# Kernel tuning notes

Hardware: AMD Instinct MI355X
Metric: run time of the kernel (lower is better)

The kernel has to match this reference:

```python
import jax, jax.numpy as jnp
import numpy as np

B, T, C = 2, 2048, 2048
NH, NKV, HD = 16, 8, 256
SOFTCAP = 50.0
ROPE_BASE = 10000.0


def setup_inputs() -> dict:
    key = jax.random.key(0)
    ks = jax.random.split(key, 5)
    s = 0.02
    return {
        "X": jax.random.normal(ks[0], (B, T, C), dtype=jnp.float32),
        "Wq": jax.random.normal(ks[1], (C, NH * HD), dtype=jnp.float32) * s,
        "Wk": jax.random.normal(ks[2], (C, NKV * HD), dtype=jnp.float32) * s,
        "Wv": jax.random.normal(ks[3], (C, NKV * HD), dtype=jnp.float32) * s,
        "Wo": jax.random.normal(ks[4], (NH * HD, C), dtype=jnp.float32) * s,
    }


def _rotate_half(x):
    x1, x2 = x[..., : x.shape[-1] // 2], x[..., x.shape[-1] // 2 :]
    return jnp.concatenate((-x2, x1), axis=-1)


def _rope_cos_sin(t, head_dim, dtype):
    inv_freq = 1.0 / ROPE_BASE ** (
        jnp.arange(0, head_dim, 2, dtype=jnp.int32).astype(jnp.float32) / head_dim
    )  # [HD/2]
    pos = jnp.arange(t, dtype=jnp.float32)  # [T]
    freqs = pos[:, None] * inv_freq[None, :]  # [T, HD/2]
    emb = jnp.concatenate((freqs, freqs), axis=-1)  # [T, HD]
    # shape [1, 1, T, HD] to broadcast over (B, H, T, HD)
    return (
        jnp.cos(emb).astype(dtype)[None, None],
        jnp.sin(emb).astype(dtype)[None, None],
    )


def reference(X, Wq, Wk, Wv, Wo):
    b, t, c = X.shape
    n_rep = NH // NKV

    q = (X @ Wq).reshape(b, t, NH, HD).transpose(0, 2, 1, 3)   # [B,NH,T,HD]
    k = (X @ Wk).reshape(b, t, NKV, HD).transpose(0, 2, 1, 3)  # [B,NKV,T,HD]
    v = (X @ Wv).reshape(b, t, NKV, HD).transpose(0, 2, 1, 3)

    cos, sin = _rope_cos_sin(t, HD, X.dtype)
    q = q * cos + _rotate_half(q) * sin
    k = k * cos + _rotate_half(k) * sin

    # repeat_kv (GQA): [B,NKV,T,HD] -> [B,NH,T,HD]
    k = jnp.repeat(k, n_rep, axis=1)
    v = jnp.repeat(v, n_rep, axis=1)

    scale = 256.0 ** (-0.5)  # hardcoded in source
    att = jnp.einsum("bhqd,bhkd->bhqk", q, k) * scale
    # tanh logit softcapping
    att = SOFTCAP * jnp.tanh(att / SOFTCAP)
    # causal mask
    causal = jnp.tril(jnp.ones((t, t), dtype=bool))
    att = jnp.where(causal[None, None], att, -jnp.inf)
    att = jax.nn.softmax(att, axis=-1)

    y = jnp.einsum("bhqk,bhkd->bhqd", att, v)  # [B,NH,T,HD]
    y = y.transpose(0, 2, 1, 3).reshape(b, t, NH * HD)
    return y @ Wo
```

## Files before the change

### kernel.cpp

```cpp
#include <hip/hip_runtime.h>
#include <hip/hip_bf16.h>

#define NHD 16
#define NKVH 8
#define HDIM 256
#define TSEQ 2048
#define BATCH 2

typedef unsigned int   u32;
typedef unsigned short u16;

typedef __attribute__((ext_vector_type(8))) short bf16x8;
typedef __attribute__((ext_vector_type(4))) float floatx4;

__device__ inline u32 cvt2bf(float lo, float hi) {
  u32 r;
  asm("v_cvt_pk_bf16_f32 %0, %1, %2" : "=v"(r) : "v"(lo), "v"(hi));
  return r;
}
__device__ inline u16 f2bf(float f) {
  union { float f; u32 i; } v; v.f = f;
  u32 r = v.i + 0x7fffu + ((v.i >> 16) & 1u);
  return (u16)(r >> 16);
}
__device__ inline float bf2f(u16 u) {
  union { u32 i; float f; } v; v.i = ((u32)u) << 16; return v.f;
}
__device__ inline float fexp2(float x) {
  float r; asm("v_exp_f32 %0, %1" : "=v"(r) : "v"(x)); return r;
}

typedef const __attribute__((address_space(1))) u32* gptr_t;
typedef __attribute__((address_space(3))) u32* lptr_t;
__device__ inline void gl_lds16(const void* g, void* l) {
  __builtin_amdgcn_global_load_lds((gptr_t)g, (lptr_t)l, 16, 0, 0);
}

__device__ inline void tconv_body(const float* __restrict__ in,
                                  u16* __restrict__ out, int R, int Cc,
                                  int bx, int by, int tid) {
  __shared__ float tile[64][65];
  const int r0 = by * 64, c0 = bx * 64;
  const int tr = tid >> 4;
  const int tc = (tid & 15) * 4;
#pragma unroll
  for (int j = 0; j < 4; ++j) {
    float4 v = *(const float4*)(in + (size_t)(r0 + tr + j * 16) * Cc + c0 + tc);
    tile[tr + j * 16][tc + 0] = v.x;
    tile[tr + j * 16][tc + 1] = v.y;
    tile[tr + j * 16][tc + 2] = v.z;
    tile[tr + j * 16][tc + 3] = v.w;
  }
  __syncthreads();
#pragma unroll
  for (int j = 0; j < 4; ++j) {
    int c = tr + j * 16;
    u16 o[4];
#pragma unroll
    for (int i = 0; i < 4; ++i) o[i] = f2bf(tile[tc + i][c]);
    *(uint2*)(out + (size_t)(c0 + c) * R + r0 + tc) = *(const uint2*)o;
  }
}

__global__ __launch_bounds__(256) void tconv_k(
    const float* __restrict__ in, u16* __restrict__ out, int R, int Cc)
{
  tconv_body(in, out, R, Cc, blockIdx.x, blockIdx.y, threadIdx.x);
}

__global__ __launch_bounds__(256) void xconv_k(
    const float* __restrict__ in, u16* __restrict__ out)
{
  size_t i = (size_t)blockIdx.x * 256 + threadIdx.x;
  float4 a = *(const float4*)(in + i * 8);
  float4 b = *(const float4*)(in + i * 8 + 4);
  uint4 o;
  o.x = cvt2bf(a.x, a.y); o.y = cvt2bf(a.z, a.w);
  o.z = cvt2bf(b.x, b.y); o.w = cvt2bf(b.z, b.w);
  *(uint4*)(out + i * 8) = o;
}

__global__ __launch_bounds__(256) void prep_k(
    const float* __restrict__ X,  const float* __restrict__ Wq,
    const float* __restrict__ Wk, const float* __restrict__ Wv,
    u16* __restrict__ XB, u16* __restrict__ WqT, u16* __restrict__ WkvT)
{
  const int bid = blockIdx.x, tid = threadIdx.x;
  if (bid < 4096) {
    size_t i = (size_t)bid * 256 + tid;
    float4 a = *(const float4*)(X + i * 8);
    float4 b = *(const float4*)(X + i * 8 + 4);
    uint4 o;
    o.x = cvt2bf(a.x, a.y); o.y = cvt2bf(a.z, a.w);
    o.z = cvt2bf(b.x, b.y); o.w = cvt2bf(b.z, b.w);
    *(uint4*)(XB + i * 8) = o;
  } else if (bid < 6144) {
    int idx = bid - 4096;
    tconv_body(Wq, WqT, 2048, 4096, idx & 63, idx >> 6, tid);
  } else if (bid < 7168) {
    int idx = bid - 6144;
    tconv_body(Wk, WkvT, 2048, 2048, idx & 31, idx >> 5, tid);
  } else {
    int idx = bid - 7168;
    tconv_body(Wv, WkvT + (size_t)2048 * 2048, 2048, 2048, idx & 31, idx >> 5, tid);
  }
}

template<int EPI, int BM>
__global__ __launch_bounds__(512, 2) void gemm256_k(
    const u16* __restrict__ Ab, const u16* __restrict__ BTp,
    void* __restrict__ Op, int M, int N, int K)
{
  constexpr int NI = BM / 32;
  constexpr int AI = BM / 64;
  __shared__ u16 LA[2][BM * 64];
  __shared__ u16 LB[2][256 * 64];
  const int t = threadIdx.x;
  const int lane = t & 63, wave = t >> 6;
  const int lg = lane >> 4, l15 = lane & 15;
  const int wm = wave >> 2, wn = wave & 3;
  const int mtiles = M / BM;
  const int mt = (int)blockIdx.x % mtiles, nt = (int)blockIdx.x / mtiles;
  const int m0 = mt * BM, n0 = nt << 8;

  const int arow = wave * (BM / 8) + (lane >> 3);
  const int ska  = ((lane & 7) ^ (arow & 7)) << 3;
  const int brow = wave * 32 + (lane >> 3);
  const int skb  = ((lane & 7) ^ (brow & 7)) << 3;
  const u16* Ag = Ab  + (size_t)(m0 + arow) * K + ska;
  const u16* Bg = BTp + (size_t)(n0 + brow) * K + skb;

  auto STAGE = [&](int k0, int sel) {
#pragma unroll
    for (int q = 0; q < AI; ++q)
      gl_lds16(Ag + k0 + (size_t)q * 8 * K, &LA[sel][(wave * (BM / 8) + q * 8) * 64]);
#pragma unroll
    for (int q = 0; q < 4; ++q)
      gl_lds16(Bg + k0 + (size_t)q * 8 * K, &LB[sel][(wave * 32 + q * 8) * 64]);
  };

  floatx4 acc[NI][4];
#pragma unroll
  for (int i = 0; i < NI; ++i)
#pragma unroll
    for (int j = 0; j < 4; ++j) acc[i][j] = (floatx4){0.f, 0.f, 0.f, 0.f};

  STAGE(0, 0);
  const int KT = K >> 6;
  for (int kt = 0; kt < KT; ++kt) {
    const int sel = kt & 1;
    if (kt + 1 < KT) {
      STAGE((kt + 1) << 6, sel ^ 1);
      if constexpr (BM == 256) asm volatile("s_waitcnt vmcnt(8)" ::: "memory");
      else                     asm volatile("s_waitcnt vmcnt(6)" ::: "memory");
    } else {
      asm volatile("s_waitcnt vmcnt(0)" ::: "memory");
    }
    __builtin_amdgcn_s_barrier();
    __builtin_amdgcn_sched_barrier(0);
    __builtin_amdgcn_s_setprio(1);
#pragma unroll
    for (int ks = 0; ks < 2; ++ks) {
      const int c = (ks << 2) + lg;
      bf16x8 bfv[4];
#pragma unroll
      for (int j = 0; j < 4; ++j) {
        int row = wn * 64 + (j << 4) + l15;
        bfv[j] = *(const bf16x8*)(&LB[sel][row * 64 + ((c ^ (row & 7)) << 3)]);
      }
#pragma unroll
      for (int i = 0; i < NI; ++i) {
        int row = wm * (BM / 2) + (i << 4) + l15;
        bf16x8 af = *(const bf16x8*)(&LA[sel][row * 64 + ((c ^ (row & 7)) << 3)]);
#pragma unroll
        for (int j = 0; j < 4; ++j)
          acc[i][j] = __builtin_amdgcn_mfma_f32_16x16x32_bf16(af, bfv[j], acc[i][j], 0, 0, 0);
      }
    }
    __builtin_amdgcn_s_setprio(0);
    __builtin_amdgcn_s_barrier();
  }

#pragma unroll
  for (int i = 0; i < NI; ++i) {
#pragma unroll
    for (int j = 0; j < 4; ++j) {
#pragma unroll
      for (int r = 0; r < 4; ++r) {
        int m = m0 + wm * (BM / 2) + (i << 4) + (lg << 2) + r;
        int n = n0 + wn * 64 + (j << 4) + l15;
        float v = acc[i][j][r];
        int bb = m >> 11, tt = m & 2047;
        if (EPI == 0) {
          ((float*)Op)[(size_t)m * N + n] = v;
        } else if (EPI == 1) {
          int h = n >> 8, d = n & 255;
          ((u16*)Op)[(((size_t)bb * NHD + h) * TSEQ + tt) * HDIM + d] = f2bf(v);
        } else {
          if (n < 2048) {
            int h = n >> 8, d = n & 255;
            ((u16*)Op)[(((size_t)bb * NKVH + h) * TSEQ + tt) * HDIM + d] = f2bf(v);
          } else {
            int n2 = n - 2048;
            int h = n2 >> 8, d = n2 & 255;
            ((u16*)Op)[8388608u + (((size_t)bb * NKVH + h) * HDIM + d) * TSEQ + tt] = f2bf(v);
          }
        }
      }
    }
  }
}

__global__ __launch_bounds__(256) void rope_k(u16* Qb, u16* Kb) {
  size_t idx = (size_t)blockIdx.x * 256 + threadIdx.x;
  const size_t qtot = (size_t)BATCH * NHD * TSEQ * 128;
  u16* buf;
  if (idx < qtot) buf = Qb;
  else { idx -= qtot; buf = Kb; }
  int d = (int)(idx & 127);
  size_t rest = idx >> 7;
  int tt = (int)(rest & (TSEQ - 1));
  float invf = exp2f(-(float)d * 0.103810253f);
  float th = (float)tt * invf;
  float sn, cs;
  sincosf(th, &sn, &cs);
  size_t base = rest * HDIM;
  float x1 = bf2f(buf[base + d]);
  float x2 = bf2f(buf[base + d + 128]);
  buf[base + d]       = f2bf(x1 * cs - x2 * sn);
  buf[base + d + 128] = f2bf(x2 * cs + x1 * sn);
}

__global__ __launch_bounds__(256, 2) void attn_k(
    const u16* __restrict__ Q, const u16* __restrict__ Kb,
    const u16* __restrict__ Vt, u16* __restrict__ Y)
{
  __shared__ u16 Ks2[2][32 * 256];
  __shared__ u16 Vs2[2][256 * 32];
  __shared__ u16 Ps[4 * 16 * 32];
  __shared__ float Ls[4][16];
  const int t = threadIdx.x, lane = t & 63, w = t >> 6;
  const int lg = lane >> 4, l15 = lane & 15;
  const int qt = 31 - (int)blockIdx.y;
  const int h = (int)blockIdx.x >> 1, b = (int)blockIdx.x & 1;
  const int hkv = h >> 1;

  const u16* Kg = Kb + ((size_t)(b * NKVH + hkv)) * TSEQ * HDIM;
  const u16* Vg = Vt + ((size_t)(b * NKVH + hkv)) * HDIM * TSEQ;

  int koff[4], voff[4];
#pragma unroll
  for (int q = 0; q < 4; ++q) {
    int krow = w * 8 + q * 2 + (lane >> 5);
    int kcc  = lane & 31;
    koff[q] = krow * 256 + ((kcc ^ (krow & 7)) << 3);
    int vd  = w * 64 + q * 16 + (lane >> 2);
    voff[q] = vd * TSEQ + (((lane & 3) ^ ((vd >> 2) & 3)) << 3);
  }

  auto STAGE = [&](int st, int sel) {
    const u16* kbase = Kg + (size_t)st * (32 * 256);
    const u16* vbase = Vg + st * 32;
#pragma unroll
    for (int q = 0; q < 4; ++q)
      gl_lds16(kbase + koff[q], &Ks2[sel][(w * 8 + q * 2) * 256]);
#pragma unroll
    for (int q = 0; q < 4; ++q)
      gl_lds16(vbase + voff[q], &Vs2[sel][(w * 64 + q * 16) * 32]);
  };

  const u16* Qg = Q + (((size_t)(b * NHD + h)) * TSEQ + qt * 64 + w * 16 + l15) * HDIM;
  bf16x8 qf[8];
#pragma unroll
  for (int ks = 0; ks < 8; ++ks) qf[ks] = *(const bf16x8*)(Qg + ks * 32 + lg * 8);

  floatx4 accY[16];
#pragma unroll
  for (int i = 0; i < 16; ++i) accY[i] = (floatx4){0.f, 0.f, 0.f, 0.f};
  float rsum = 0.f;

  const int qglob = qt * 64 + w * 16 + l15;
  const int qmaxw = qt * 64 + w * 16 + 15;
  const int nst = 2 * qt + 2;
  const int fps = (l15 ^ (l15 >> 2)) & 3;

  STAGE(0, 0);
  for (int st = 0; st < nst; ++st) {
    const int sel = st & 1;
    if (st + 1 < nst) {
      STAGE(st + 1, sel ^ 1);
      asm volatile("s_waitcnt vmcnt(8)" ::: "memory");
    } else {
      asm volatile("s_waitcnt vmcnt(0)" ::: "memory");
    }
    __builtin_amdgcn_s_barrier();
    __builtin_amdgcn_sched_barrier(0);

    if (st * 32 <= qmaxw) {
      __builtin_amdgcn_s_setprio(1);
#pragma unroll
      for (int stile = 0; stile < 2; ++stile) {
        floatx4 sa0 = (floatx4){0.f, 0.f, 0.f, 0.f};
        floatx4 sa1 = (floatx4){0.f, 0.f, 0.f, 0.f};
#pragma unroll
        for (int ks = 0; ks < 8; ++ks) {
          int row = (stile << 4) + l15;
          int c = (ks << 2) + lg;
          bf16x8 kf = *(const bf16x8*)((const char*)Ks2[sel] +
                        row * 512 + ((c ^ (row & 7)) << 4));
          if (ks & 1)
            sa1 = __builtin_amdgcn_mfma_f32_16x16x32_bf16(kf, qf[ks], sa1, 0, 0, 0);
          else
            sa0 = __builtin_amdgcn_mfma_f32_16x16x32_bf16(kf, qf[ks], sa0, 0, 0, 0);
        }
        int sbase = st * 32 + (stile << 4) + (lg << 2);
        float p[4];
#pragma unroll
        for (int r = 0; r < 4; ++r) {
          float s = sa0[r] + sa1[r];
          float tt = fmaf(s * s, -5.2083333e-7f, 1.0f);
          float pv = fexp2(s * 0.0901684403f * tt);
          pv = (sbase + r <= qglob) ? pv : 0.0f;
          p[r] = pv;
          rsum += pv;
        }
        uint2 pw;
        pw.x = cvt2bf(p[0], p[1]);
        pw.y = cvt2bf(p[2], p[3]);
        int o = (stile << 5) + (lg << 3);
        int gran = (o >> 4) ^ fps;
        *(uint2*)((char*)Ps + (w << 10) + l15 * 64 + (gran << 4) + (o & 15)) = pw;
      }
      {
        bf16x8 pf = *(const bf16x8*)((const char*)Ps + (w << 10) + l15 * 64 +
                      ((lg ^ fps) << 4));
#pragma unroll
        for (int dt = 0; dt < 16; ++dt) {
          int row = (dt << 4) + l15;
          bf16x8 vf = *(const bf16x8*)((const char*)Vs2[sel] +
                        row * 64 + ((lg ^ ((row >> 2) & 3)) << 4));
          accY[dt] = __builtin_amdgcn_mfma_f32_16x16x32_bf16(pf, vf, accY[dt], 0, 0, 0);
        }
      }
      __builtin_amdgcn_s_setprio(0);
    }
    __builtin_amdgcn_s_barrier();
  }

  rsum += __shfl_xor(rsum, 16);
  rsum += __shfl_xor(rsum, 32);
  if (lane < 16) Ls[w][l15] = rsum;
  __syncthreads();
  float inv[4];
#pragma unroll
  for (int r = 0; r < 4; ++r) inv[r] = 1.0f / Ls[w][(lg << 2) + r];

  u16* Yg = Y + ((size_t)(b * TSEQ + qt * 64 + w * 16)) * (NHD * HDIM) + h * HDIM;
#pragma unroll
  for (int dt = 0; dt < 16; ++dt)
#pragma unroll
    for (int r = 0; r < 4; ++r)
      Yg[(size_t)((lg << 2) + r) * (NHD * HDIM) + (dt << 4) + l15] =
          f2bf(accY[dt][r] * inv[r]);
}

extern "C" void kernel_launch(void* const* d_in, const int* in_sizes, int n_in,
                              void* d_out, int out_size, void* d_ws, size_t ws_size,
                              hipStream_t stream) {
  const float* X  = (const float*)d_in[0];
  const float* Wq = (const float*)d_in[1];
  const float* Wk = (const float*)d_in[2];
  const float* Wv = (const float*)d_in[3];
  const float* Wo = (const float*)d_in[4];
  float* out = (float*)d_out;

  u16* ws = (u16*)d_ws;
  dim3 blk(256);

  if (ws_size >= (size_t)117440512) {
    u16* XB   = ws;
    u16* WqT  = ws + 8388608;
    u16* WkvT = ws + 16777216;
    u16* Qb   = ws + 25165824;
    u16* KVb  = ws + 41943040;
    u16* Yb   = ws;
    u16* WoT  = ws + 25165824;

    prep_k<<<dim3(8192), blk, 0, stream>>>(X, Wq, Wk, Wv, XB, WqT, WkvT);
    gemm256_k<1, 256><<<dim3(256), dim3(512), 0, stream>>>(XB, WqT,  Qb,  4096, 4096, 2048);
    gemm256_k<3, 256><<<dim3(256), dim3(512), 0, stream>>>(XB, WkvT, KVb, 4096, 4096, 2048);
    rope_k<<<dim3(49152), blk, 0, stream>>>(Qb, KVb);
    attn_k<<<dim3(32, 32), blk, 0, stream>>>(Qb, KVb, KVb + 8388608, Yb);
    tconv_k<<<dim3(32, 64), blk, 0, stream>>>(Wo, WoT, 4096, 2048);
    gemm256_k<0, 128><<<dim3(256), dim3(512), 0, stream>>>(Yb, WoT, out, 4096, 2048, 4096);
  } else {
    u16* XB   = ws;
    u16* WT   = ws + 8388608;
    u16* Qb   = ws + 16777216;
    u16* KVb  = ws + 33554432;
    u16* Yb   = ws;
    u16* WoT  = ws + 16777216;

    xconv_k<<<dim3(4096), blk, 0, stream>>>(X, XB);
    tconv_k<<<dim3(64, 32), blk, 0, stream>>>(Wq, WT, 2048, 4096);
    gemm256_k<1, 256><<<dim3(256), dim3(512), 0, stream>>>(XB, WT, Qb, 4096, 4096, 2048);
    tconv_k<<<dim3(32, 32), blk, 0, stream>>>(Wk, WT, 2048, 2048);
    tconv_k<<<dim3(32, 32), blk, 0, stream>>>(Wv, WT + (size_t)2048 * 2048, 2048, 2048);
    gemm256_k<3, 256><<<dim3(256), dim3(512), 0, stream>>>(XB, WT, KVb, 4096, 4096, 2048);
    rope_k<<<dim3(49152), blk, 0, stream>>>(Qb, KVb);
    attn_k<<<dim3(32, 32), blk, 0, stream>>>(Qb, KVb, KVb + 8388608, Yb);
    tconv_k<<<dim3(32, 64), blk, 0, stream>>>(Wo, WoT, 4096, 2048);
    gemm256_k<0, 128><<<dim3(256), dim3(512), 0, stream>>>(Yb, WoT, out, 4096, 2048, 4096);
  }
}
```

Measured before the change: 419.7 us.

## Fuse RoPE into Q/KV projection GEMM epilogue and drop separate rope kernel

The separate rope_k pass over Q and K is removed, and the rotation is applied in the projection GEMM epilogue. The B-tile column mapping is remapped so that each wave holds dimension pairs d and d+128 in its accumulators, and sin/cos come from hardware v_sin/v_cos on a fractional revolution. This saves one full read and write of Q and K in bf16 plus a kernel launch. The price is extra epilogue ALU work and lower-precision hardware trig, which could affect accuracy at large positions.

New measurement: 398.4 us. -5.1%, faster.

```diff
diff --git a/kernel.cpp b/kernel.cpp
--- a/kernel.cpp
+++ b/kernel.cpp
@@ -28,6 +28,15 @@
 }
 __device__ inline float fexp2(float x) {
   float r; asm("v_exp_f32 %0, %1" : "=v"(r) : "v"(x)); return r;
+}
+__device__ inline float fsin(float x) {
+  float r; asm("v_sin_f32 %0, %1" : "=v"(r) : "v"(x)); return r;
+}
+__device__ inline float fcos(float x) {
+  float r; asm("v_cos_f32 %0, %1" : "=v"(r) : "v"(x)); return r;
+}
+__device__ inline float ffract(float x) {
+  float r; asm("v_fract_f32 %0, %1" : "=v"(r) : "v"(x)); return r;
 }
 
 typedef const __attribute__((address_space(1))) u32* gptr_t;
@@ -165,7 +174,8 @@
       bf16x8 bfv[4];
 #pragma unroll
       for (int j = 0; j < 4; ++j) {
-        int row = wn * 64 + (j << 4) + l15;
+        int row = (EPI == 0) ? (wn * 64 + (j << 4) + l15)
+                             : (wn * 32 + ((j & 1) << 4) + ((j >> 1) << 7) + l15);
         bfv[j] = *(const bf16x8*)(&LB[sel][row * 64 + ((c ^ (row & 7)) << 3)]);
       }
 #pragma unroll
@@ -181,54 +191,66 @@
     __builtin_amdgcn_s_barrier();
   }
 
-#pragma unroll
-  for (int i = 0; i < NI; ++i) {
-#pragma unroll
-    for (int j = 0; j < 4; ++j) {
-#pragma unroll
-      for (int r = 0; r < 4; ++r) {
-        int m = m0 + wm * (BM / 2) + (i << 4) + (lg << 2) + r;
-        int n = n0 + wn * 64 + (j << 4) + l15;
-        float v = acc[i][j][r];
-        int bb = m >> 11, tt = m & 2047;
-        if (EPI == 0) {
-          ((float*)Op)[(size_t)m * N + n] = v;
-        } else if (EPI == 1) {
-          int h = n >> 8, d = n & 255;
-          ((u16*)Op)[(((size_t)bb * NHD + h) * TSEQ + tt) * HDIM + d] = f2bf(v);
-        } else {
-          if (n < 2048) {
-            int h = n >> 8, d = n & 255;
-            ((u16*)Op)[(((size_t)bb * NKVH + h) * TSEQ + tt) * HDIM + d] = f2bf(v);
+  if constexpr (EPI == 0) {
+#pragma unroll
+    for (int i = 0; i < NI; ++i)
+#pragma unroll
+      for (int j = 0; j < 4; ++j)
+#pragma unroll
+        for (int r = 0; r < 4; ++r) {
+          int m = m0 + wm * (BM / 2) + (i << 4) + (lg << 2) + r;
+          int n = n0 + wn * 64 + (j << 4) + l15;
+          ((float*)Op)[(size_t)m * N + n] = acc[i][j][r];
+        }
+  } else {
+    float invf2[2];
+#pragma unroll
+    for (int j = 0; j < 2; ++j) {
+      int col = wn * 32 + (j << 4) + l15;
+      invf2[j] = fexp2(fmaf(-(float)col, 0.103810253f, -2.651496129f));
+    }
+#pragma unroll
+    for (int i = 0; i < NI; ++i) {
+#pragma unroll
+      for (int j = 0; j < 2; ++j) {
+        int col = wn * 32 + (j << 4) + l15;
+        int n_lo = n0 + col;
+#pragma unroll
+        for (int r = 0; r < 4; ++r) {
+          int m = m0 + wm * (BM / 2) + (i << 4) + (lg << 2) + r;
+          int bb = m >> 11, tt = m & 2047;
+          float vlo = acc[i][j][r], vhi = acc[i][j + 2][r];
+          if (EPI == 1 || n_lo < 2048) {
+            float rev = ffract((float)tt * invf2[j]);
+            float sn = fsin(rev), cs = fcos(rev);
+            float olo = vlo * cs - vhi * sn;
+            float ohi = vhi * cs + vlo * sn;
+            vlo = olo; vhi = ohi;
+          }
+          if (EPI == 1) {
+            int h = n_lo >> 8;
+            u16* dst = (u16*)Op + (((size_t)bb * NHD + h) * TSEQ + tt) * HDIM + col;
+            dst[0]   = f2bf(vlo);
+            dst[128] = f2bf(vhi);
           } else {
-            int n2 = n - 2048;
-            int h = n2 >> 8, d = n2 & 255;
-            ((u16*)Op)[8388608u + (((size_t)bb * NKVH + h) * HDIM + d) * TSEQ + tt] = f2bf(v);
+            if (n_lo < 2048) {
+              int h = n_lo >> 8;
+              u16* dst = (u16*)Op + (((size_t)bb * NKVH + h) * TSEQ + tt) * HDIM + col;
+              dst[0]   = f2bf(vlo);
+              dst[128] = f2bf(vhi);
+            } else {
+              int n2 = n_lo - 2048;
+              int h = n2 >> 8;
+              u16* dst = (u16*)Op + 8388608u +
+                         (((size_t)bb * NKVH + h) * HDIM + col) * TSEQ + tt;
+              dst[0] = f2bf(vlo);
+              dst[(size_t)128 * TSEQ] = f2bf(vhi);
+            }
           }
         }
       }
     }
   }
-}
-
-__global__ __launch_bounds__(256) void rope_k(u16* Qb, u16* Kb) {
-  size_t idx = (size_t)blockIdx.x * 256 + threadIdx.x;
-  const size_t qtot = (size_t)BATCH * NHD * TSEQ * 128;
-  u16* buf;
-  if (idx < qtot) buf = Qb;
-  else { idx -= qtot; buf = Kb; }
-  int d = (int)(idx & 127);
-  size_t rest = idx >> 7;
-  int tt = (int)(rest & (TSEQ - 1));
-  float invf = exp2f(-(float)d * 0.103810253f);
-  float th = (float)tt * invf;
-  float sn, cs;
-  sincosf(th, &sn, &cs);
-  size_t base = rest * HDIM;
-  float x1 = bf2f(buf[base + d]);
-  float x2 = bf2f(buf[base + d + 128]);
-  buf[base + d]       = f2bf(x1 * cs - x2 * sn);
-  buf[base + d + 128] = f2bf(x2 * cs + x1 * sn);
 }
 
 __global__ __launch_bounds__(256, 2) void attn_k(
@@ -389,7 +411,6 @@
     prep_k<<<dim3(8192), blk, 0, stream>>>(X, Wq, Wk, Wv, XB, WqT, WkvT);
     gemm256_k<1, 256><<<dim3(256), dim3(512), 0, stream>>>(XB, WqT,  Qb,  4096, 4096, 2048);
     gemm256_k<3, 256><<<dim3(256), dim3(512), 0, stream>>>(XB, WkvT, KVb, 4096, 4096, 2048);
-    rope_k<<<dim3(49152), blk, 0, stream>>>(Qb, KVb);
     attn_k<<<dim3(32, 32), blk, 0, stream>>>(Qb, KVb, KVb + 8388608, Yb);
     tconv_k<<<dim3(32, 64), blk, 0, stream>>>(Wo, WoT, 4096, 2048);
     gemm256_k<0, 128><<<dim3(256), dim3(512), 0, stream>>>(Yb, WoT, out, 4096, 2048, 4096);
@@ -407,7 +428,6 @@
     tconv_k<<<dim3(32, 32), blk, 0, stream>>>(Wk, WT, 2048, 2048);
     tconv_k<<<dim3(32, 32), blk, 0, stream>>>(Wv, WT + (size_t)2048 * 2048, 2048, 2048);
     gemm256_k<3, 256><<<dim3(256), dim3(512), 0, stream>>>(XB, WT, KVb, 4096, 4096, 2048);
-    rope_k<<<dim3(49152), blk, 0, stream>>>(Qb, KVb);
     attn_k<<<dim3(32, 32), blk, 0, stream>>>(Qb, KVb, KVb + 8388608, Yb);
     tconv_k<<<dim3(32, 64), blk, 0, stream>>>(Wo, WoT, 4096, 2048);
     gemm256_k<0, 128><<<dim3(256), dim3(512), 0, stream>>>(Yb, WoT, out, 4096, 2048, 4096);
```
